# Performance work log

Hardware: AMD Instinct MI355X
Metric: run time of the kernel (lower is better)

Reference implementation:

```python
import jax, jax.numpy as jnp
import numpy as np

NUM_HEADS = 4
KERNEL = 4
EPS = 1e-6


def _causal_conv1d(x, w, b):
    # x: (B,S,D), w: (D,1,K) depthwise, b: (D,)
    xc = x.transpose(0, 2, 1)  # (B,D,S)
    y = jax.lax.conv_general_dilated(
        xc, w, window_strides=(1,), padding=[(w.shape[-1] - 1, 0)],
        feature_group_count=xc.shape[1])
    return (y + b[None, :, None]).transpose(0, 2, 1)  # (B,S,D)


def _headwise(x, w):
    # x: (B,S,D), w: (NH, DH_out, DH_in) block-diagonal linear, no bias
    B, S, D = x.shape
    nh, dout, din = w.shape
    xh = x.reshape(B, S, nh, din)
    return jnp.einsum('bshd,hod->bsho', xh, w).reshape(B, S, nh * dout)


def _slstm_scan(gates, R, b):
    # gates: (B,S,4,NH,DH) ordered [i,f,z,o]; R: (NH,DH,4*DH); b: (4,NH,DH)
    B, S, _, nh, dh = gates.shape
    gseq = gates.transpose(1, 0, 2, 3, 4)  # (S,B,4,NH,DH)
    zero = jnp.zeros((B, nh, dh), gates.dtype)
    init = (zero, zero, zero, zero)  # h, c, n, m

    def step(carry, g):
        h, c, n, m = carry
        rec = jnp.einsum('bhd,hdk->bhk', h, R)
        rec = rec.reshape(B, nh, 4, dh).transpose(0, 2, 1, 3)  # (B,4,NH,DH)
        raw = g + rec + b[None]
        iraw, fraw, zraw, oraw = raw[:, 0], raw[:, 1], raw[:, 2], raw[:, 3]
        logfplusm = m + jax.nn.log_sigmoid(fraw)
        m_new = jnp.maximum(iraw, logfplusm)  # stabilizer
        ig = jnp.exp(iraw - m_new)
        fg = jnp.exp(logfplusm - m_new)
        c_new = fg * c + ig * jnp.tanh(zraw)
        n_new = fg * n + ig
        h_new = jax.nn.sigmoid(oraw) * c_new / n_new
        return (h_new, c_new, n_new, m_new), h_new

    _, ys = jax.lax.scan(step, init, gseq)  # ys: (S,B,NH,DH)
    return ys.transpose(1, 2, 0, 3)  # (B,NH,S,DH)


def _multihead_layernorm(y, scale, bias):
    # y: (B,NH,S,DH); normalize over DH per head
    mu = y.mean(-1, keepdims=True)
    var = y.var(-1, keepdims=True)
    yn = (y - mu) * jax.lax.rsqrt(var + EPS)
    nh, dh = y.shape[1], y.shape[3]
    return yn * scale.reshape(1, nh, 1, dh) + bias.reshape(1, nh, 1, dh)


def setup_inputs() -> dict:
    key = jax.random.key(0)
    ks = jax.random.split(key, 12)
    B, S, D = 4, 2048, 1024
    nh, dh = NUM_HEADS, D // NUM_HEADS
    sd_conv = 1.0 / np.sqrt(KERNEL)
    sd_head = 1.0 / np.sqrt(dh)
    return {
        'x': jax.random.normal(ks[0], (B, S, D), jnp.float32),
        'conv_w': jax.random.normal(ks[1], (D, 1, KERNEL), jnp.float32) * sd_conv,
        'conv_b': jnp.zeros((D,), jnp.float32),
        'w_i': jax.random.normal(ks[2], (nh, dh, dh), jnp.float32) * sd_head,
        'w_f': jax.random.normal(ks[3], (nh, dh, dh), jnp.float32) * sd_head,
        'w_z': jax.random.normal(ks[4], (nh, dh, dh), jnp.float32) * sd_head,
        'w_o': jax.random.normal(ks[5], (nh, dh, dh), jnp.float32) * sd_head,
        'rec_kernel': jax.random.normal(ks[6], (nh, dh, 4 * dh), jnp.float32) * sd_head,
        'cell_bias': jnp.zeros((4, nh, dh), jnp.float32),
        'gn_scale': jnp.ones((D,), jnp.float32),
        'gn_bias': jnp.zeros((D,), jnp.float32),
    }


def reference(x, conv_w, conv_b, w_i, w_f, w_z, w_o, rec_kernel, cell_bias, gn_scale, gn_bias):
    B, S, D = x.shape
    dh = D // NUM_HEADS
    x_conv = jax.nn.swish(_causal_conv1d(x, conv_w, conv_b))
    i = _headwise(x_conv, w_i)
    f = _headwise(x_conv, w_f)
    z = _headwise(x, w_z)
    o = _headwise(x, w_o)
    # concat order [i,f,z,o]; reshape to (B,S,4,NH,DH)
    gates = jnp.stack([i, f, z, o], axis=2).reshape(B, S, 4, NUM_HEADS, dh)
    y = _slstm_scan(gates, rec_kernel, cell_bias)  # (B,NH,S,DH)
    out = _multihead_layernorm(y, gn_scale, gn_bias)
    return out.transpose(0, 2, 1, 3).reshape(B, S, D)
```

## Files before the change

kernel.cpp:

```cpp
#include <hip/hip_runtime.h>
#include <hip/hip_bf16.h>

#define NH 4
#define DH 256
#define DMODEL 1024
#define BB 4
#define SS 2048

typedef __attribute__((ext_vector_type(4))) float f32x4;
typedef __attribute__((ext_vector_type(8))) short bf16x8;
typedef __attribute__((ext_vector_type(4))) int i32x4;

__device__ __forceinline__ int dot4i8(int acc, int a, int b) {
#if __has_builtin(__builtin_amdgcn_sdot4)
    return __builtin_amdgcn_sdot4(a, b, acc, false);
#else
#pragma unroll
    for (int i = 0; i < 4; ++i) {
        int av = (a << (24 - 8 * i)) >> 24;
        int bv = (b << (24 - 8 * i)) >> 24;
        acc += av * bv;
    }
    return acc;
#endif
}

__device__ __forceinline__ void wg_barrier() {
    asm volatile("s_waitcnt lgkmcnt(0)" ::: "memory");
    __builtin_amdgcn_s_barrier();
    __builtin_amdgcn_sched_barrier(0);
}

__global__ void k_conv(const float* __restrict__ x, const float* __restrict__ cw,
                       const float* __restrict__ cb, float* __restrict__ xc) {
    int bs = blockIdx.x;
    int s = bs & (SS - 1);
    const float* xrow = x + (size_t)bs * DMODEL;
#pragma unroll
    for (int dd = 0; dd < 4; ++dd) {
        int d = threadIdx.x + dd * 256;
        float w0 = cw[d * 4 + 0], w1 = cw[d * 4 + 1], w2 = cw[d * 4 + 2], w3 = cw[d * 4 + 3];
        float acc = cb[d] + w3 * xrow[d];
        if (s >= 1) acc += w2 * xrow[d - DMODEL];
        if (s >= 2) acc += w1 * xrow[d - 2 * DMODEL];
        if (s >= 3) acc += w0 * xrow[d - 3 * DMODEL];
        float sig = 1.f / (1.f + __expf(-acc));
        xc[(size_t)bs * DMODEL + d] = acc * sig;
    }
}

__global__ void k_gemm(const float* __restrict__ x, const float* __restrict__ xc,
                       const float* __restrict__ wi, const float* __restrict__ wf,
                       const float* __restrict__ wz, const float* __restrict__ wo,
                       float* __restrict__ gates) {
    int h = blockIdx.z >> 1, pair = blockIdx.z & 1;
    const float* A = pair ? x : xc;
    int n0 = blockIdx.y * 64;
    const float* W = (n0 < 256) ? (pair ? wz : wi) : (pair ? wo : wf);
    int nl = n0 & 255;
    int m0 = blockIdx.x * 64;

    __shared__ __align__(16) __hip_bfloat16 Al[64][72];
    __shared__ __align__(16) __hip_bfloat16 Bl[64][72];

    int tid = threadIdx.x;
    int lane = tid & 63, wv = tid >> 6;
    f32x4 acc[4] = {};

    for (int k0 = 0; k0 < 256; k0 += 64) {
        __syncthreads();
#pragma unroll
        for (int i = 0; i < 4; ++i) {
            int f4 = tid + i * 256;
            int r = f4 >> 4, c4 = (f4 & 15) * 4;
            const float* srcA = A + (size_t)(m0 + r) * DMODEL + h * DH + k0 + c4;
            float4 v = *(const float4*)srcA;
            Al[r][c4 + 0] = __float2bfloat16(v.x);
            Al[r][c4 + 1] = __float2bfloat16(v.y);
            Al[r][c4 + 2] = __float2bfloat16(v.z);
            Al[r][c4 + 3] = __float2bfloat16(v.w);
            const float* srcB = W + (size_t)(h * DH + nl + r) * DH + k0 + c4;
            float4 u = *(const float4*)srcB;
            Bl[r][c4 + 0] = __float2bfloat16(u.x);
            Bl[r][c4 + 1] = __float2bfloat16(u.y);
            Bl[r][c4 + 2] = __float2bfloat16(u.z);
            Bl[r][c4 + 3] = __float2bfloat16(u.w);
        }
        __syncthreads();
#pragma unroll
        for (int kk = 0; kk < 64; kk += 32) {
            bf16x8 a = *(const bf16x8*)&Al[wv * 16 + (lane & 15)][kk + (lane >> 4) * 8];
#pragma unroll
            for (int nt = 0; nt < 4; ++nt) {
                bf16x8 bfr = *(const bf16x8*)&Bl[nt * 16 + (lane & 15)][kk + (lane >> 4) * 8];
                acc[nt] = __builtin_amdgcn_mfma_f32_16x16x32_bf16(a, bfr, acc[nt], 0, 0, 0);
            }
        }
    }
#pragma unroll
    for (int nt = 0; nt < 4; ++nt)
#pragma unroll
        for (int r = 0; r < 4; ++r) {
            int m = m0 + wv * 16 + (lane >> 4) * 4 + r;
            int n = n0 + nt * 16 + (lane & 15);
            int b = m >> 11, s = m & (SS - 1);
            int g = pair * 2 + (n >> 8), d = n & 255;
            gates[((((size_t)(b * NH + h)) * SS + s) * 4 + g) * DH + d] = acc[nt][r];
        }
}

__global__ void k_prep(const float* __restrict__ R, int* __restrict__ Wq,
                       float* __restrict__ scales) {
    int colid = blockIdx.x * 4 + (threadIdx.x >> 6);
    int lane = threadIdx.x & 63;
    int h = colid >> 10, k = colid & 1023;
    const float* base = R + (size_t)h * 256 * 1024 + k;
    float v[4];
    float mx = 0.f;
#pragma unroll
    for (int i = 0; i < 4; ++i) {
        v[i] = base[(size_t)(lane * 4 + i) * 1024];
        mx = fmaxf(mx, fabsf(v[i]));
    }
    for (int off = 32; off; off >>= 1) mx = fmaxf(mx, __shfl_xor(mx, off));
    mx = fmaxf(mx, 1e-30f);
    float scale = mx * (1.f / 127.f);
    float inv = 127.f / mx;
    int pk = 0;
#pragma unroll
    for (int i = 0; i < 4; ++i) {
        int q = (int)rintf(v[i] * inv);
        q = max(-127, min(127, q));
        pk |= (q & 255) << (8 * i);
    }
    Wq[(h * 64 + lane) * 1024 + k] = pk;
    if (lane == 0) scales[h * 1024 + k] = scale;
}

__launch_bounds__(256, 1)
__global__ void k_scan(const float* __restrict__ gates, const int* __restrict__ Wq,
                       const float* __restrict__ scales, const float* __restrict__ bias,
                       float* __restrict__ y) {
    int bh = blockIdx.x;
    int h = bh & 3;
    int d = threadIdx.x;
    int lane = d & 63;
    int wv = d >> 6;
    int kg = lane >> 4;
    int cl = lane & 15;

    __shared__ __align__(16) signed char hq[2][256];

    int wf[64], wz[64], wo[64];
#pragma unroll
    for (int j = 0; j < 64; ++j) {
        const int* row = Wq + (size_t)(h * 64 + j) * 1024 + d;
        wf[j] = row[256];
        wz[j] = row[512];
        wo[j] = row[768];
    }

    i32x4 bfr[4][4];
#pragma unroll
    for (int tt = 0; tt < 4; ++tt) {
        int col = wv * 64 + tt * 16 + cl;
#pragma unroll
        for (int c = 0; c < 4; ++c)
#pragma unroll
            for (int j4 = 0; j4 < 4; ++j4)
                bfr[tt][c][j4] = Wq[(h * 64 + c * 16 + kg * 4 + j4) * 1024 + col];
    }
    i32x4 acc[4];
#pragma unroll
    for (int tt = 0; tt < 4; ++tt) acc[tt] = (i32x4){0, 0, 0, 0};

    float cmi = scales[h * 1024 + d] * (1.f / 127.f);
    float cmf = scales[h * 1024 + 256 + d] * (1.f / 127.f);
    float cmz = scales[h * 1024 + 512 + d] * (1.f / 127.f);
    float cmo = scales[h * 1024 + 768 + d] * (1.f / 127.f);
    float bi = bias[(0 * NH + h) * DH + d];
    float bf_ = bias[(1 * NH + h) * DH + d];
    float bz = bias[(2 * NH + h) * DH + d];
    float bo = bias[(3 * NH + h) * DH + d];

    float c_ = 0.f, n_ = 0.f, mstate = 0.f;
    const float* gbase = gates + (size_t)bh * SS * 1024;
    float* ybase = y + (size_t)bh * SS * DH;

    if (d < 32) ((i32x4*)hq)[d] = (i32x4){0, 0, 0, 0};
    __syncthreads();

    float gA0 = gbase[d], gA1 = gbase[256 + d], gA2 = gbase[512 + d], gA3 = gbase[768 + d];
    float gB0 = gbase[1024 + d], gB1 = gbase[1024 + 256 + d];
    float gB2 = gbase[1024 + 512 + d], gB3 = gbase[1024 + 768 + d];

#define DOT3(JJ, HV)                  \
    af = dot4i8(af, wf[JJ], (HV));    \
    az = dot4i8(az, wz[JJ], (HV));    \
    ao = dot4i8(ao, wo[JJ], (HV));

#define SCAN_STEP(P, G0, G1, G2, G3, SCUR)                                     \
    {                                                                          \
        int sp = (SCUR) + 2 < SS ? (SCUR) + 2 : SS - 1;                        \
        const float* gp = gbase + (size_t)sp * 1024 + d;                       \
        float p0 = gp[0], p1 = gp[256], p2 = gp[512], p3 = gp[768];            \
        const i32x4* hp = (const i32x4*)hq[P];                                 \
                                    \
        i32x4 a0 = hp[kg], a1 = hp[4 + kg], a2 = hp[8 + kg], a3 = hp[12 + kg]; \
        acc[0].x = 0; acc[1].x = 0; acc[2].x = 0; acc[3].x = 0;                \
        _Pragma("unroll") for (int tt = 0; tt < 4; ++tt)                       \
            acc[tt] = __builtin_amdgcn_mfma_i32_16x16x64_i8(a0, bfr[tt][0], acc[tt], 0, 0, 0); \
        _Pragma("unroll") for (int tt = 0; tt < 4; ++tt)                       \
            acc[tt] = __builtin_amdgcn_mfma_i32_16x16x64_i8(a1, bfr[tt][1], acc[tt], 0, 0, 0); \
        _Pragma("unroll") for (int tt = 0; tt < 4; ++tt)                       \
            acc[tt] = __builtin_amdgcn_mfma_i32_16x16x64_i8(a2, bfr[tt][2], acc[tt], 0, 0, 0); \
        _Pragma("unroll") for (int tt = 0; tt < 4; ++tt)                       \
            acc[tt] = __builtin_amdgcn_mfma_i32_16x16x64_i8(a3, bfr[tt][3], acc[tt], 0, 0, 0); \
                 \
        int af = 0, az = 0, ao = 0;                                            \
        _Pragma("unroll") for (int cc = 0; cc < 4; ++cc) {                     \
            i32x4 h0 = hp[cc * 4 + 0], h1 = hp[cc * 4 + 1];                    \
            i32x4 h2 = hp[cc * 4 + 2], h3 = hp[cc * 4 + 3];                    \
            DOT3(cc * 16 + 0, h0.x)  DOT3(cc * 16 + 1, h0.y)                   \
            DOT3(cc * 16 + 2, h0.z)  DOT3(cc * 16 + 3, h0.w)                   \
            DOT3(cc * 16 + 4, h1.x)  DOT3(cc * 16 + 5, h1.y)                   \
            DOT3(cc * 16 + 6, h1.z)  DOT3(cc * 16 + 7, h1.w)                   \
            DOT3(cc * 16 + 8, h2.x)  DOT3(cc * 16 + 9, h2.y)                   \
            DOT3(cc * 16 + 10, h2.z) DOT3(cc * 16 + 11, h2.w)                  \
            DOT3(cc * 16 + 12, h3.x) DOT3(cc * 16 + 13, h3.y)                  \
            DOT3(cc * 16 + 14, h3.z) DOT3(cc * 16 + 15, h3.w)                  \
        }                                                                      \
               \
        int s0 = __shfl(acc[0].x, cl);                                         \
        int s1 = __shfl(acc[1].x, cl);                                         \
        int s2 = __shfl(acc[2].x, cl);                                         \
        int s3 = __shfl(acc[3].x, cl);                                         \
        int v01 = (d & 16) ? s1 : s0;                                          \
        int v23 = (d & 16) ? s3 : s2;                                          \
        int ri_raw = (d & 32) ? v23 : v01;                                     \
        float rawi = (G0) + (float)ri_raw * cmi + bi;                          \
        float rawf = (G1) + (float)af * cmf + bf_;                             \
        float rawz = (G2) + (float)az * cmz + bz;                              \
        float rawo = (G3) + (float)ao * cmo + bo;                              \
        float lsf = fminf(rawf, 0.f) - __logf(1.f + __expf(-fabsf(rawf)));     \
        float lfm = mstate + lsf;                                              \
        float mn = fmaxf(rawi, lfm);                                           \
        float ig = __expf(rawi - mn);                                          \
        float fg = __expf(lfm - mn);                                           \
        float az_ = fabsf(rawz);                                               \
        float e2 = __expf(-2.f * az_);                                         \
        float th = (1.f - e2) / (1.f + e2);                                    \
        th = rawz < 0.f ? -th : th;                                            \
        c_ = fg * c_ + ig * th;                                                \
        n_ = fg * n_ + ig;                                                     \
        mstate = mn;                                                           \
        float so = 1.f / (1.f + __expf(-rawo));                                \
        float hv = so * c_ / n_;                                               \
        ybase[(size_t)(SCUR)*DH + d] = hv;                                     \
        hq[(P) ^ 1][d] = (signed char)(int)rintf(hv * 127.f);                  \
        G0 = p0; G1 = p1; G2 = p2; G3 = p3;                                    \
        wg_barrier();                                                          \
    }

    for (int s = 0; s < SS; s += 2) {
        SCAN_STEP(0, gA0, gA1, gA2, gA3, s)
        SCAN_STEP(1, gB0, gB1, gB2, gB3, s + 1)
    }
#undef SCAN_STEP
#undef DOT3
}

__global__ void k_ln(const float* __restrict__ y, const float* __restrict__ gsc,
                     const float* __restrict__ gbi, float* __restrict__ out) {
    int bid = blockIdx.x;
    int s = bid & (SS - 1);
    int bh = bid >> 11;
    int b = bh >> 2, h = bh & 3;
    int d = threadIdx.x;
    float v = y[(size_t)bid * DH + d];
    float s1 = v, s2 = v * v;
    for (int off = 32; off; off >>= 1) {
        s1 += __shfl_xor(s1, off);
        s2 += __shfl_xor(s2, off);
    }
    __shared__ float a1[4], a2[4];
    int wv = threadIdx.x >> 6, ln = threadIdx.x & 63;
    if (ln == 0) { a1[wv] = s1; a2[wv] = s2; }
    __syncthreads();
    s1 = a1[0] + a1[1] + a1[2] + a1[3];
    s2 = a2[0] + a2[1] + a2[2] + a2[3];
    float mu = s1 * (1.f / 256.f);
    float var = s2 * (1.f / 256.f) - mu * mu;
    float rs = rsqrtf(var + 1e-6f);
    float o = (v - mu) * rs * gsc[h * DH + d] + gbi[h * DH + d];
    out[((size_t)(b * SS + s)) * DMODEL + h * DH + d] = o;
}

extern "C" void kernel_launch(void* const* d_in, const int* in_sizes, int n_in,
                              void* d_out, int out_size, void* d_ws, size_t ws_size,
                              hipStream_t stream) {
    (void)in_sizes; (void)n_in; (void)out_size; (void)ws_size;
    const float* x = (const float*)d_in[0];
    const float* cw = (const float*)d_in[1];
    const float* cb = (const float*)d_in[2];
    const float* wi = (const float*)d_in[3];
    const float* wf = (const float*)d_in[4];
    const float* wz = (const float*)d_in[5];
    const float* wo = (const float*)d_in[6];
    const float* R = (const float*)d_in[7];
    const float* cbias = (const float*)d_in[8];
    const float* gsc = (const float*)d_in[9];
    const float* gbi = (const float*)d_in[10];
    float* out = (float*)d_out;

    char* ws = (char*)d_ws;
    float* xc = (float*)ws;
    float* gates = (float*)(ws + 33554432ull);
    float* yb = (float*)(ws + 167772160ull);
    int* Wq = (int*)(ws + 201326592ull);
    float* scales = (float*)(ws + 202375168ull);

    k_prep<<<1024, 256, 0, stream>>>(R, Wq, scales);
    k_conv<<<BB * SS, 256, 0, stream>>>(x, cw, cb, xc);
    k_gemm<<<dim3(128, 8, 8), 256, 0, stream>>>(x, xc, wi, wf, wz, wo, gates);
    k_scan<<<16, 256, 0, stream>>>(gates, Wq, scales, cbias, yb);
    k_ln<<<BB * SS * NH, 256, 0, stream>>>(yb, gsc, gbi, out);
}
```

Baseline: 2.304 ms.

## Split scan recurrence across 512 threads with MFMA for i/f and lane-split dot for z/o

The sLSTM scan block doubles from 256 to 512 threads (8 waves), each wave owning 32 hidden units. The i and f gate recurrences go through int8 MFMA tiles. The z and o gates are split across wave halves, each doing a 64-term dot4 with h broadcast via readlane, which replaces the per-thread triple dot over all of h. This cuts the serial per-step dot work and register pressure per thread, in exchange for more waves hitting the per-step barrier and extra shuffles. Half of each wave's lanes compute redundant gate math and are masked on stores.

```diff
diff --git a/kernel.cpp b/kernel.cpp
--- a/kernel.cpp
+++ b/kernel.cpp
@@ -137,42 +137,41 @@
     if (lane == 0) scales[h * 1024 + k] = scale;
 }
 
-__launch_bounds__(256, 1)
+__launch_bounds__(512, 2)
 __global__ void k_scan(const float* __restrict__ gates, const int* __restrict__ Wq,
                        const float* __restrict__ scales, const float* __restrict__ bias,
                        float* __restrict__ y) {
     int bh = blockIdx.x;
     int h = bh & 3;
-    int d = threadIdx.x;
-    int lane = d & 63;
-    int wv = d >> 6;
-    int kg = lane >> 4;
-    int cl = lane & 15;
+    int t = threadIdx.x;
+    int l = t & 63;
+    int wv = t >> 6;
+    int kg = l >> 4;
+    int cl = l & 15;
+    int lz = l & 31;
+    int d = wv * 32 + lz;
 
     __shared__ __align__(16) signed char hq[2][256];
 
-    int wf[64], wz[64], wo[64];
-#pragma unroll
-    for (int j = 0; j < 64; ++j) {
-        const int* row = Wq + (size_t)(h * 64 + j) * 1024 + d;
-        wf[j] = row[256];
-        wz[j] = row[512];
-        wo[j] = row[768];
-    }
-
     i32x4 bfr[4][4];
 #pragma unroll
-    for (int tt = 0; tt < 4; ++tt) {
-        int col = wv * 64 + tt * 16 + cl;
+    for (int ti = 0; ti < 4; ++ti) {
+        int g = ti >> 1, tt = ti & 1;
+        int col = g * 256 + wv * 32 + tt * 16 + cl;
 #pragma unroll
         for (int c = 0; c < 4; ++c)
 #pragma unroll
             for (int j4 = 0; j4 < 4; ++j4)
-                bfr[tt][c][j4] = Wq[(h * 64 + c * 16 + kg * 4 + j4) * 1024 + col];
+                bfr[ti][c][j4] = Wq[(h * 64 + c * 16 + kg * 4 + j4) * 1024 + col];
     }
     i32x4 acc[4];
 #pragma unroll
-    for (int tt = 0; tt < 4; ++tt) acc[tt] = (i32x4){0, 0, 0, 0};
+    for (int ti = 0; ti < 4; ++ti) acc[ti] = (i32x4){0, 0, 0, 0};
+
+    int dotcol = (l < 32) ? (512 + wv * 32 + l) : (768 + wv * 32 + (l - 32));
+    int w[64];
+#pragma unroll
+    for (int j = 0; j < 64; ++j) w[j] = Wq[(h * 64 + j) * 1024 + dotcol];
 
     float cmi = scales[h * 1024 + d] * (1.f / 127.f);
     float cmf = scales[h * 1024 + 256 + d] * (1.f / 127.f);
@@ -187,61 +186,58 @@
     const float* gbase = gates + (size_t)bh * SS * 1024;
     float* ybase = y + (size_t)bh * SS * DH;
 
-    if (d < 32) ((i32x4*)hq)[d] = (i32x4){0, 0, 0, 0};
+    if (t < 32) ((i32x4*)hq)[t] = (i32x4){0, 0, 0, 0};
     __syncthreads();
 
-    float gA0 = gbase[d], gA1 = gbase[256 + d], gA2 = gbase[512 + d], gA3 = gbase[768 + d];
-    float gB0 = gbase[1024 + d], gB1 = gbase[1024 + 256 + d];
-    float gB2 = gbase[1024 + 512 + d], gB3 = gbase[1024 + 768 + d];
-
-#define DOT3(JJ, HV)                  \
-    af = dot4i8(af, wf[JJ], (HV));    \
-    az = dot4i8(az, wz[JJ], (HV));    \
-    ao = dot4i8(ao, wo[JJ], (HV));
+    float gA0 = 0, gA1 = 0, gA2 = 0, gA3 = 0, gB0 = 0, gB1 = 0, gB2 = 0, gB3 = 0;
+    if (l < 32) {
+        gA0 = gbase[d]; gA1 = gbase[256 + d]; gA2 = gbase[512 + d]; gA3 = gbase[768 + d];
+        gB0 = gbase[1024 + d]; gB1 = gbase[1024 + 256 + d];
+        gB2 = gbase[1024 + 512 + d]; gB3 = gbase[1024 + 768 + d];
+    }
 
 #define SCAN_STEP(P, G0, G1, G2, G3, SCUR)                                     \
     {                                                                          \
-        int sp = (SCUR) + 2 < SS ? (SCUR) + 2 : SS - 1;                        \
-        const float* gp = gbase + (size_t)sp * 1024 + d;                       \
-        float p0 = gp[0], p1 = gp[256], p2 = gp[512], p3 = gp[768];            \
+        float p0 = 0, p1 = 0, p2 = 0, p3 = 0;                                  \
+        if (l < 32) {                                                          \
+            int sp = (SCUR) + 2 < SS ? (SCUR) + 2 : SS - 1;                    \
+            const float* gp = gbase + (size_t)sp * 1024 + d;                   \
+            p0 = gp[0]; p1 = gp[256]; p2 = gp[512]; p3 = gp[768];              \
+        }                                                                      \
         const i32x4* hp = (const i32x4*)hq[P];                                 \
-                                    \
+        int hflat = ((const int*)hq[P])[l];                                    \
+                                       \
         i32x4 a0 = hp[kg], a1 = hp[4 + kg], a2 = hp[8 + kg], a3 = hp[12 + kg]; \
         acc[0].x = 0; acc[1].x = 0; acc[2].x = 0; acc[3].x = 0;                \
-        _Pragma("unroll") for (int tt = 0; tt < 4; ++tt)                       \
-            acc[tt] = __builtin_amdgcn_mfma_i32_16x16x64_i8(a0, bfr[tt][0], acc[tt], 0, 0, 0); \
-        _Pragma("unroll") for (int tt = 0; tt < 4; ++tt)                       \
-            acc[tt] = __builtin_amdgcn_mfma_i32_16x16x64_i8(a1, bfr[tt][1], acc[tt], 0, 0, 0); \
-        _Pragma("unroll") for (int tt = 0; tt < 4; ++tt)                       \
-            acc[tt] = __builtin_amdgcn_mfma_i32_16x16x64_i8(a2, bfr[tt][2], acc[tt], 0, 0, 0); \
-        _Pragma("unroll") for (int tt = 0; tt < 4; ++tt)                       \
-            acc[tt] = __builtin_amdgcn_mfma_i32_16x16x64_i8(a3, bfr[tt][3], acc[tt], 0, 0, 0); \
-                 \
-        int af = 0, az = 0, ao = 0;                                            \
-        _Pragma("unroll") for (int cc = 0; cc < 4; ++cc) {                     \
-            i32x4 h0 = hp[cc * 4 + 0], h1 = hp[cc * 4 + 1];                    \
-            i32x4 h2 = hp[cc * 4 + 2], h3 = hp[cc * 4 + 3];                    \
-            DOT3(cc * 16 + 0, h0.x)  DOT3(cc * 16 + 1, h0.y)                   \
-            DOT3(cc * 16 + 2, h0.z)  DOT3(cc * 16 + 3, h0.w)                   \
-            DOT3(cc * 16 + 4, h1.x)  DOT3(cc * 16 + 5, h1.y)                   \
-            DOT3(cc * 16 + 6, h1.z)  DOT3(cc * 16 + 7, h1.w)                   \
-            DOT3(cc * 16 + 8, h2.x)  DOT3(cc * 16 + 9, h2.y)                   \
-            DOT3(cc * 16 + 10, h2.z) DOT3(cc * 16 + 11, h2.w)                  \
-            DOT3(cc * 16 + 12, h3.x) DOT3(cc * 16 + 13, h3.y)                  \
-            DOT3(cc * 16 + 14, h3.z) DOT3(cc * 16 + 15, h3.w)                  \
+        _Pragma("unroll") for (int ti = 0; ti < 4; ++ti)                       \
+            acc[ti] = __builtin_amdgcn_mfma_i32_16x16x64_i8(a0, bfr[ti][0], acc[ti], 0, 0, 0); \
+        _Pragma("unroll") for (int ti = 0; ti < 4; ++ti)                       \
+            acc[ti] = __builtin_amdgcn_mfma_i32_16x16x64_i8(a1, bfr[ti][1], acc[ti], 0, 0, 0); \
+        _Pragma("unroll") for (int ti = 0; ti < 4; ++ti)                       \
+            acc[ti] = __builtin_amdgcn_mfma_i32_16x16x64_i8(a2, bfr[ti][2], acc[ti], 0, 0, 0); \
+        _Pragma("unroll") for (int ti = 0; ti < 4; ++ti)                       \
+            acc[ti] = __builtin_amdgcn_mfma_i32_16x16x64_i8(a3, bfr[ti][3], acc[ti], 0, 0, 0); \
+          \
+        int da0 = 0, da1 = 0, da2 = 0, da3 = 0;                                \
+        _Pragma("unroll") for (int j = 0; j < 64; j += 4) {                    \
+            da0 = dot4i8(da0, __builtin_amdgcn_readlane(hflat, j + 0), w[j + 0]); \
+            da1 = dot4i8(da1, __builtin_amdgcn_readlane(hflat, j + 1), w[j + 1]); \
+            da2 = dot4i8(da2, __builtin_amdgcn_readlane(hflat, j + 2), w[j + 2]); \
+            da3 = dot4i8(da3, __builtin_amdgcn_readlane(hflat, j + 3), w[j + 3]); \
         }                                                                      \
-               \
-        int s0 = __shfl(acc[0].x, cl);                                         \
-        int s1 = __shfl(acc[1].x, cl);                                         \
-        int s2 = __shfl(acc[2].x, cl);                                         \
-        int s3 = __shfl(acc[3].x, cl);                                         \
-        int v01 = (d & 16) ? s1 : s0;                                          \
-        int v23 = (d & 16) ? s3 : s2;                                          \
-        int ri_raw = (d & 32) ? v23 : v01;                                     \
+        int adot = (da0 + da1) + (da2 + da3);                                  \
+             \
+        int ri0 = __shfl(acc[0].x, cl);                                        \
+        int ri1 = __shfl(acc[1].x, cl);                                        \
+        int rf0 = __shfl(acc[2].x, cl);                                        \
+        int rf1 = __shfl(acc[3].x, cl);                                        \
+        int roX = __shfl(adot, l | 32);                                        \
+        int ri_raw = (l & 16) ? ri1 : ri0;                                     \
+        int rf_raw = (l & 16) ? rf1 : rf0;                                     \
         float rawi = (G0) + (float)ri_raw * cmi + bi;                          \
-        float rawf = (G1) + (float)af * cmf + bf_;                             \
-        float rawz = (G2) + (float)az * cmz + bz;                              \
-        float rawo = (G3) + (float)ao * cmo + bo;                              \
+        float rawf = (G1) + (float)rf_raw * cmf + bf_;                         \
+        float rawz = (G2) + (float)adot * cmz + bz;                            \
+        float rawo = (G3) + (float)roX * cmo + bo;                             \
         float lsf = fminf(rawf, 0.f) - __logf(1.f + __expf(-fabsf(rawf)));     \
         float lfm = mstate + lsf;                                              \
         float mn = fmaxf(rawi, lfm);                                           \
@@ -256,8 +252,10 @@
         mstate = mn;                                                           \
         float so = 1.f / (1.f + __expf(-rawo));                                \
         float hv = so * c_ / n_;                                               \
-        ybase[(size_t)(SCUR)*DH + d] = hv;                                     \
-        hq[(P) ^ 1][d] = (signed char)(int)rintf(hv * 127.f);                  \
+        if (l < 32) {                                                          \
+            ybase[(size_t)(SCUR)*DH + d] = hv;                                 \
+            hq[(P) ^ 1][d] = (signed char)(int)rintf(hv * 127.f);              \
+        }                                                                      \
         G0 = p0; G1 = p1; G2 = p2; G3 = p3;                                    \
         wg_barrier();                                                          \
     }
@@ -267,7 +265,6 @@
         SCAN_STEP(1, gB0, gB1, gB2, gB3, s + 1)
     }
 #undef SCAN_STEP
-#undef DOT3
 }
 
 __global__ void k_ln(const float* __restrict__ y, const float* __restrict__ gsc,
@@ -323,6 +320,6 @@
     k_prep<<<1024, 256, 0, stream>>>(R, Wq, scales);
     k_conv<<<BB * SS, 256, 0, stream>>>(x, cw, cb, xc);
     k_gemm<<<dim3(128, 8, 8), 256, 0, stream>>>(x, xc, wi, wf, wz, wo, gates);
-    k_scan<<<16, 256, 0, stream>>>(gates, Wq, scales, cbias, yb);
+    k_scan<<<16, 512, 0, stream>>>(gates, Wq, scales, cbias, yb);
     k_ln<<<BB * SS * NH, 256, 0, stream>>>(yb, gsc, gbi, out);
 }
```

New measurement: 3.126 ms. 35.7% more time.
